# Kernel optimization log

Hardware: AMD Instinct MI355X
Metric: run time of the kernel (lower is better)

The kernel has to match this reference:

```python
import jax, jax.numpy as jnp
import numpy as np

EMBED_DIM = 1024
NUM_HEADS = 16
HEAD_DIM = EMBED_DIM // NUM_HEADS
SCALE = HEAD_DIM ** -0.5


def setup_inputs() -> dict:
    key = jax.random.key(0)
    k1, k2, k3, k4, k5, k6 = jax.random.split(key, 6)
    B, Tq, Tk = 2, 2048, 2048
    std = EMBED_DIM ** -0.5
    return {
        "x_q": jax.random.normal(k1, (B, Tq, EMBED_DIM), jnp.float32),
        "x_kv": jax.random.normal(k2, (B, Tk, EMBED_DIM), jnp.float32),
        "w_q": jax.random.normal(k3, (EMBED_DIM, EMBED_DIM), jnp.float32) * std,
        "w_kv": jax.random.normal(k4, (EMBED_DIM, 2 * EMBED_DIM), jnp.float32) * std,
        "w_proj": jax.random.normal(k5, (EMBED_DIM, EMBED_DIM), jnp.float32) * std,
        "w_rel": jax.random.normal(k6, (1, NUM_HEADS), jnp.float32) * 0.02,
    }


def reference(x_q, x_kv, w_q, w_kv, w_proj, w_rel):
    B, Tq, _ = x_q.shape
    Tk = x_kv.shape[1]
    # projections
    q = x_q @ w_q                       # [B,Tq,E]
    kv = x_kv @ w_kv                    # [B,Tk,2E]
    k, v = jnp.split(kv, 2, axis=-1)

    def heads(y, T):
        return y.reshape(B, T, NUM_HEADS, HEAD_DIM).transpose(0, 2, 1, 3)

    q = heads(q, Tq)                    # [B,H,Tq,D]
    k = heads(k, Tk)
    v = heads(v, Tk)

    logits = jnp.einsum('bhqd,bhkd->bhqk', q, k) * SCALE  # [B,H,Tq,Tk]

    # relative position bias: Dense(1 -> H) applied to (pos_q - pos_k)
    rel = jnp.arange(Tq, dtype=jnp.float32)[:, None] - jnp.arange(Tk, dtype=jnp.float32)[None, :]
    bias = rel[..., None] * w_rel[0]                      # [Tq,Tk,H]
    bias = bias.transpose(2, 0, 1)[None]                  # [1,H,Tq,Tk]
    logits = logits + bias

    attn = jax.nn.softmax(logits, axis=-1)                # dropout=0 / inference -> identity
    out = jnp.einsum('bhqk,bhkd->bhqd', attn, v)          # [B,H,Tq,D]
    out = out.transpose(0, 2, 1, 3).reshape(B, Tq, EMBED_DIM)
    return out @ w_proj
```

## Files before the change

kernel.cpp:

```cpp
#include <hip/hip_runtime.h>
#include <hip/hip_bf16.h>

typedef __attribute__((ext_vector_type(8))) short short8;
typedef __attribute__((ext_vector_type(8))) __bf16 bf16x8;
typedef __attribute__((ext_vector_type(4))) float f32x4;
typedef __attribute__((ext_vector_type(8))) unsigned short ushort8v;
typedef __attribute__((ext_vector_type(4))) unsigned short ushort4v;

#define NB 2
#define TQ 2048
#define TKK 2048
#define EMB 1024
#define NH 16
#define HD 64

__device__ __forceinline__ unsigned short f2bf(float f){
  union { float f; unsigned u; } v; v.f = f;
  unsigned r = v.u + 0x7FFFu + ((v.u >> 16) & 1u);
  return (unsigned short)(r >> 16);
}

#define GLOAD_LDS16(g, l) __builtin_amdgcn_global_load_lds( \
    (const __attribute__((address_space(1))) void*)(g), \
    (__attribute__((address_space(3))) void*)(l), 16, 0, 0)

#define SWZ(row, inner) ((inner) ^ (((row)&7)<<4))

__device__ __forceinline__ void mfma16(const short8& a, const short8& b, f32x4& c){
  c = __builtin_amdgcn_mfma_f32_16x16x32_bf16(
        __builtin_bit_cast(bf16x8, a), __builtin_bit_cast(bf16x8, b), c, 0, 0, 0);
}

__device__ __forceinline__ void cvt_body(const float* __restrict__ in,
    unsigned short* __restrict__ out, int i){
  float4 v = ((const float4*)in)[i];
  ushort4v o;
  o.x = f2bf(v.x); o.y = f2bf(v.y); o.z = f2bf(v.z); o.w = f2bf(v.w);
  ((ushort4v*)out)[i] = o;
}

__device__ __forceinline__ void wt_body(const float* __restrict__ W,
    unsigned short* __restrict__ WT, int K, int N, int k0, int n0,
    unsigned short (*tile)[72]){
  int tid = threadIdx.x;
  #pragma unroll
  for (int it=0; it<4; ++it){
    int c = tid + it*256;
    int r = c>>4, c4 = (c&15)*4;
    float4 v = *(const float4*)(W + (long)(k0+r)*N + n0 + c4);
    tile[r][c4+0]=f2bf(v.x); tile[r][c4+1]=f2bf(v.y);
    tile[r][c4+2]=f2bf(v.z); tile[r][c4+3]=f2bf(v.w);
  }
  __syncthreads();
  #pragma unroll
  for (int it=0; it<2; ++it){
    int c = tid + it*256;
    int n = c>>3, k8 = (c&7)*8;
    ushort8v o;
    #pragma unroll
    for (int j=0;j<8;++j) o[j] = tile[k8+j][n];
    *(ushort8v*)(WT + (long)(n0+n)*K + k0 + k8) = o;
  }
}

__global__ __launch_bounds__(256) void prep_kernel(
    const float* __restrict__ x_q, const float* __restrict__ x_kv,
    const float* __restrict__ w_q, const float* __restrict__ w_kv,
    const float* __restrict__ w_proj,
    unsigned short* __restrict__ Aq,  unsigned short* __restrict__ Akv,
    unsigned short* __restrict__ WqT, unsigned short* __restrict__ WkvT,
    unsigned short* __restrict__ WpT){
  __shared__ unsigned short tile[64][72];
  const int bx = blockIdx.x;
  if (bx < 4096){
    cvt_body(x_q, Aq, bx*256 + threadIdx.x);
  } else if (bx < 8192){
    cvt_body(x_kv, Akv, (bx-4096)*256 + threadIdx.x);
  } else if (bx < 8448){
    int blk = bx - 8192;
    wt_body(w_q, WqT, EMB, EMB, (blk>>4)*64, (blk&15)*64, tile);
  } else if (bx < 8960){
    int blk = bx - 8448;
    wt_body(w_kv, WkvT, EMB, 2*EMB, (blk>>5)*64, (blk&31)*64, tile);
  } else {
    int blk = bx - 8960;
    wt_body(w_proj, WpT, EMB, EMB, (blk>>4)*64, (blk&15)*64, tile);
  }
}

template<int MODE>
__device__ __forceinline__ void gemm_body(const unsigned short* __restrict__ A,
    const unsigned short* __restrict__ BT, void* __restrict__ Cout,
    int M, int N, int K, int m0, int n0,
    unsigned short* Al, unsigned short* Bl, const float* __restrict__ w_rel){
  const int tid = threadIdx.x;
  const int wave = tid>>6, lane = tid&63;
  const int wm = (wave>>1)*64, wn = (wave&1)*64;
  const int g = lane>>4, lr = lane&15;
  const int srow = lane>>3;
  const int sinner = (lane&7)*16;
  f32x4 acc[4][4] = {};

  for (int k0=0; k0<K; k0+=64){
    #pragma unroll
    for (int j=0;j<4;++j){
      int chunk = wave*4 + j;
      int row = chunk*8 + srow;
      int kb = SWZ(row, sinner);
      GLOAD_LDS16(A + (long)(m0+row)*K + k0 + (kb>>1), Al + chunk*512);
      GLOAD_LDS16(BT + (long)(n0+row)*K + k0 + (kb>>1), Bl + chunk*512);
    }
    __syncthreads();
    #pragma unroll
    for (int kk=0;kk<2;++kk){
      short8 af[4], bfr[4];
      const int kbyte = kk*64 + g*16;
      #pragma unroll
      for (int i=0;i<4;++i){
        int ar = wm + i*16 + lr;
        af[i] = *(const short8*)((const char*)Al + ar*128 + SWZ(ar, kbyte));
        int br = wn + i*16 + lr;
        bfr[i] = *(const short8*)((const char*)Bl + br*128 + SWZ(br, kbyte));
      }
      #pragma unroll
      for (int i=0;i<4;++i)
        #pragma unroll
        for (int jn=0;jn<4;++jn)
          mfma16(af[i], bfr[jn], acc[i][jn]);
    }
    __syncthreads();
  }
  #pragma unroll
  for (int i=0;i<4;++i){
    int row = m0 + wm + i*16 + g*4;
    #pragma unroll
    for (int jn=0;jn<4;++jn){
      if (MODE == 2){
        int dg = n0 - EMB + wn + jn*16 + lr;
        int h = dg >> 6, d = dg & 63;
        int b = row >> 11, t = row & (TKK-1);
        float wr2h = w_rel[h]*1.44269504f;
        float fac = exp2f(-(float)(t & 63)*wr2h);
        float stp = exp2f(-wr2h);
        ushort4v w;
        #pragma unroll
        for (int r=0;r<4;++r){ w[r] = f2bf(acc[i][jn][r]*fac); fac *= stp; }
        *(ushort4v*)((unsigned short*)Cout + ((long)((b*NH + h)*HD + d)*TKK + t)) = w;
      } else {
        int col = n0 + wn + jn*16 + lr;
        #pragma unroll
        for (int r=0;r<4;++r){
          if (MODE == 1)
            ((unsigned short*)Cout)[(long)(row+r)*N + col] = f2bf(acc[i][jn][r]);
          else
            ((float*)Cout)[(long)(row+r)*N + col] = acc[i][jn][r];
        }
      }
    }
  }
}

__global__ __launch_bounds__(256,3) void gemm_qkv(
    const unsigned short* __restrict__ Aq,  const unsigned short* __restrict__ WqT,  unsigned short* __restrict__ Qb,
    const unsigned short* __restrict__ Akv, const unsigned short* __restrict__ WkvT,
    unsigned short* __restrict__ Kb, unsigned short* __restrict__ VT,
    const float* __restrict__ w_rel){
  __shared__ unsigned short Al[128*64];
  __shared__ unsigned short Bl[128*64];
  const int p = blockIdx.x + 24*blockIdx.y;
  const int x = (p & 7) + 8*((p >> 3) % 3);
  const int y = (p >> 3) / 3;
  if (x < 8)
    gemm_body<1>(Aq,  WqT,  Qb, NB*TQ, EMB, EMB, y*128, x*128, Al, Bl, nullptr);
  else if (x < 16)
    gemm_body<1>(Akv, WkvT, Kb, NB*TKK, EMB, EMB, y*128, (x-8)*128, Al, Bl, nullptr);
  else
    gemm_body<2>(Akv, WkvT, VT, NB*TKK, EMB, EMB, y*128, EMB + (x-16)*128, Al, Bl, w_rel);
}

__global__ __launch_bounds__(256,2) void gemm_out(const unsigned short* __restrict__ A,
    const unsigned short* __restrict__ BT, float* __restrict__ C,
    int M, int N, int K){
  __shared__ unsigned short Al[64*64];
  __shared__ unsigned short Bl[128*64];
  const int tid = threadIdx.x;
  const int wave = tid>>6, lane = tid&63;
  const int m0 = blockIdx.y*64, n0 = blockIdx.x*128;
  const int wm = (wave>>1)*32, wn = (wave&1)*64;
  const int g = lane>>4, lr = lane&15;
  const int srow = lane>>3;
  const int sinner = (lane&7)*16;
  f32x4 acc[2][4] = {};

  for (int k0=0; k0<K; k0+=64){
    #pragma unroll
    for (int j=0;j<2;++j){
      int chunk = wave*2 + j;
      int row = chunk*8 + srow;
      int kb = SWZ(row, sinner);
      GLOAD_LDS16(A + (long)(m0+row)*K + k0 + (kb>>1), Al + chunk*512);
    }
    #pragma unroll
    for (int j=0;j<4;++j){
      int chunk = wave*4 + j;
      int row = chunk*8 + srow;
      int kb = SWZ(row, sinner);
      GLOAD_LDS16(BT + (long)(n0+row)*K + k0 + (kb>>1), Bl + chunk*512);
    }
    __syncthreads();
    #pragma unroll
    for (int kk=0;kk<2;++kk){
      short8 af[2], bfr[4];
      const int kbyte = kk*64 + g*16;
      #pragma unroll
      for (int i=0;i<2;++i){
        int ar = wm + i*16 + lr;
        af[i] = *(const short8*)((const char*)Al + ar*128 + SWZ(ar, kbyte));
      }
      #pragma unroll
      for (int jn=0;jn<4;++jn){
        int br = wn + jn*16 + lr;
        bfr[jn] = *(const short8*)((const char*)Bl + br*128 + SWZ(br, kbyte));
      }
      #pragma unroll
      for (int i=0;i<2;++i)
        #pragma unroll
        for (int jn=0;jn<4;++jn)
          mfma16(af[i], bfr[jn], acc[i][jn]);
    }
    __syncthreads();
  }
  #pragma unroll
  for (int i=0;i<2;++i){
    int row = m0 + wm + i*16 + g*4;
    #pragma unroll
    for (int jn=0;jn<4;++jn){
      int col = n0 + wn + jn*16 + lr;
      #pragma unroll
      for (int r=0;r<4;++r)
        C[(long)(row+r)*N + col] = acc[i][jn][r];
    }
  }
}

__global__ __launch_bounds__(512,4) void attn_kernel(const unsigned short* __restrict__ Qb,
    const unsigned short* __restrict__ Kb, const unsigned short* __restrict__ VT,
    const float* __restrict__ w_rel, unsigned short* __restrict__ Ob){
  __shared__ unsigned short Kl[3][64*64];
  __shared__ unsigned short Vl[3][64*64];
  __shared__ __attribute__((aligned(16))) char Pl[8][16*128];
  const int id  = blockIdx.x + 16*blockIdx.y;
  const int nid = (id & 7)*64 + (id >> 3);
  const int qb  = nid & 15, bh = nid >> 4;
  const int b = bh>>4, h = bh&15;
  const int q0 = qb*128;
  const int tid = threadIdx.x, wave = tid>>6, lane = tid&63;
  const int g = lane>>4, lr = lane&15;
  const int srow = lane>>3, sinner = (lane&7)*16;
  const float C1 = 0.125f*1.44269504f;
  const float wr2 = w_rel[h]*1.44269504f;
  const float w64 = 64.0f*wr2;
  char* Pw = &Pl[wave][0];

  const int strow = wave*8 + srow;
  const int skb = SWZ(strow, sinner);
  const unsigned short* Kg = Kb + (long)(b*TKK + strow)*EMB + h*HD + (skb>>1);
  const unsigned short* Vg = VT + (long)(bh*HD + strow)*TKK + (skb>>1);

  short8 qf[2];
  #pragma unroll
  for (int kk=0;kk<2;++kk)
    qf[kk] = *(const short8*)(Qb + (long)(b*TQ + q0 + wave*16 + lr)*EMB + h*HD + kk*32 + g*8);

  short8 cfrag[2];
  #pragma unroll
  for (int kk=0;kk<2;++kk)
    #pragma unroll
    for (int j=0;j<8;++j)
      cfrag[kk][j] = (short)f2bf(exp2f(-(float)(kk*32 + g*8 + j)*wr2));

  f32x4 oacc[4] = {};
  f32x4 lacc = {};
  float Mxs = -1e30f;

  GLOAD_LDS16(Kg, &Kl[0][wave*512]);
  GLOAD_LDS16(Vg, &Vl[0][wave*512]);
  GLOAD_LDS16(Kg + (long)64*EMB, &Kl[1][wave*512]);
  GLOAD_LDS16(Vg + 64, &Vl[1][wave*512]);
  asm volatile("s_waitcnt vmcnt(2)" ::: "memory");
  __builtin_amdgcn_s_barrier();

  int cur = 0;
  for (int kt=0; kt<TKK; kt+=64){
    const bool issue = (kt + 128 < TKK);
    int nxt2 = cur + 2; if (nxt2 >= 3) nxt2 -= 3;
    if (issue){
      GLOAD_LDS16(Kg + (long)(kt+128)*EMB, &Kl[nxt2][wave*512]);
      GLOAD_LDS16(Vg + (kt+128), &Vl[nxt2][wave*512]);
    }

    f32x4 sacc[4] = {};
    __builtin_amdgcn_s_setprio(1);
    #pragma unroll
    for (int kk=0;kk<2;++kk){
      short8 kf[4];
      const int kbyte = kk*64 + g*16;
      #pragma unroll
      for (int n=0;n<4;++n){
        int trow = n*16 + lr;
        kf[n] = *(const short8*)((const char*)&Kl[cur][0] + trow*128 + SWZ(trow, kbyte));
      }
      #pragma unroll
      for (int n=0;n<4;++n)
        mfma16(kf[n], qf[kk], sacc[n]);
    }
    __builtin_amdgcn_s_setprio(0);

    float rowmax;
    {
      float m0 = fmaxf(fmaxf(sacc[0][0],sacc[0][1]),sacc[0][2]);
      float m1 = fmaxf(fmaxf(sacc[0][3],sacc[1][0]),sacc[1][1]);
      float m2 = fmaxf(fmaxf(sacc[1][2],sacc[1][3]),sacc[2][0]);
      float m3 = fmaxf(fmaxf(sacc[2][1],sacc[2][2]),sacc[2][3]);
      float m4 = fmaxf(fmaxf(sacc[3][0],sacc[3][1]),sacc[3][2]);
      float a  = fmaxf(fmaxf(m0,m1),m2);
      float bb = fmaxf(fmaxf(m3,m4),sacc[3][3]);
      rowmax = fmaxf(a,bb);
      rowmax = fmaxf(rowmax, __shfl_xor(rowmax, 16, 64));
      rowmax = fmaxf(rowmax, __shfl_xor(rowmax, 32, 64));
    }
    float rowmax_s = rowmax*C1;

    if (__any(rowmax_s > Mxs + 8.0f)){
      float Mn = fmaxf(Mxs, rowmax_s);
      float rf = exp2f(Mxs - Mn);
      Mxs = Mn;
      float rfo[4];
      #pragma unroll
      for (int r=0;r<4;++r) rfo[r] = __shfl(rf, 4*g + r, 64);
      #pragma unroll
      for (int n=0;n<4;++n)
        #pragma unroll
        for (int r=0;r<4;++r) oacc[n][r] *= rfo[r];
      #pragma unroll
      for (int r=0;r<4;++r) lacc[r] *= rfo[r];
    }

    #pragma unroll
    for (int n=0;n<4;++n){
      ushort4v w;
      #pragma unroll
      for (int r=0;r<4;++r)
        w[r] = __builtin_bit_cast(unsigned short,
                 __float2bfloat16(exp2f(fmaf(sacc[n][r], C1, -Mxs))));
      *(ushort4v*)(Pw + lr*128 + SWZ(lr, 32*n + 8*g)) = w;
    }

    asm volatile("" ::: "memory");

    __builtin_amdgcn_s_setprio(1);
    #pragma unroll
    for (int kk=0;kk<2;++kk){
      const int kbyte = kk*64 + g*16;
      short8 pf = *(const short8*)(Pw + lr*128 + SWZ(lr, kbyte));
      #pragma unroll
      for (int n=0;n<4;++n){
        int vrow = n*16 + lr;
        short8 vf = *(const short8*)((const char*)&Vl[cur][0] + vrow*128 + SWZ(vrow, kbyte));
        mfma16(pf, vf, oacc[n]);
      }
      mfma16(pf, cfrag[kk], lacc);
    }
    __builtin_amdgcn_s_setprio(0);

    Mxs += w64;

    if (issue) asm volatile("s_waitcnt vmcnt(2) lgkmcnt(0)" ::: "memory");
    else       asm volatile("s_waitcnt vmcnt(0) lgkmcnt(0)" ::: "memory");
    __builtin_amdgcn_s_barrier();
    cur += 1; if (cur >= 3) cur -= 3;
  }

  #pragma unroll
  for (int r=0;r<4;++r){
    float inv = 1.0f / lacc[r];
    int q = q0 + wave*16 + 4*g + r;
    #pragma unroll
    for (int n=0;n<4;++n){
      int d = n*16 + lr;
      Ob[(long)(b*TQ + q)*EMB + h*HD + d] = f2bf(oacc[n][r]*inv);
    }
  }
}

extern "C" void kernel_launch(void* const* d_in, const int* in_sizes, int n_in,
                              void* d_out, int out_size, void* d_ws, size_t ws_size,
                              hipStream_t stream){
  const float* x_q    = (const float*)d_in[0];
  const float* x_kv   = (const float*)d_in[1];
  const float* w_q    = (const float*)d_in[2];
  const float* w_kv   = (const float*)d_in[3];
  const float* w_proj = (const float*)d_in[4];
  const float* w_rel  = (const float*)d_in[5];
  (void)in_sizes; (void)n_in; (void)out_size; (void)ws_size;
  char* ws = (char*)d_ws;
  const size_t MB = 1024*1024;
  unsigned short* Qb   = (unsigned short*)(ws + 0);
  unsigned short* Kb   = (unsigned short*)(ws + 8*MB);
  unsigned short* VT   = (unsigned short*)(ws + 16*MB);
  unsigned short* WpT  = (unsigned short*)(ws + 24*MB);
  unsigned short* WqT  = (unsigned short*)(ws + 26*MB);
  unsigned short* WkvT = (unsigned short*)(ws + 28*MB);
  unsigned short* Aq   = (unsigned short*)(ws + 32*MB);
  unsigned short* Akv  = (unsigned short*)(ws + 40*MB);
  unsigned short* Ob   = Aq;
  float* out = (float*)d_out;

  prep_kernel<<<9216, 256, 0, stream>>>(x_q, x_kv, w_q, w_kv, w_proj,
                                        Aq, Akv, WqT, WkvT, WpT);
  gemm_qkv<<<dim3(24,32), 256, 0, stream>>>(Aq, WqT, Qb, Akv, WkvT, Kb, VT, w_rel);
  attn_kernel<<<dim3(16,32), 512, 0, stream>>>(Qb, Kb, VT, w_rel, Ob);
  gemm_out<<<dim3(8,64), 256, 0, stream>>>(Ob, WpT, out, NB*TQ, EMB, EMB);
}
```

Before: 144.6 us.

## Give each attention wave two 16-row query tiles to reuse K/V fragments

The attention block now runs 4 waves of 256 threads instead of 8, and each wave handles 32 query rows as two 16-row tiles. Each K and V fragment read from LDS feeds two MFMAs, which halves LDS traffic per MFMA. Online softmax state is duplicated per tile, and each wave now issues twice as many global-to-LDS loads. The cost is more registers per wave and fewer waves per block, so latency hiding and occupancy may suffer.

```diff
diff --git a/kernel.cpp b/kernel.cpp
--- a/kernel.cpp
+++ b/kernel.cpp
@@ -243,12 +243,12 @@
   }
 }
 
-__global__ __launch_bounds__(512,4) void attn_kernel(const unsigned short* __restrict__ Qb,
+__global__ __launch_bounds__(256,2) void attn_kernel(const unsigned short* __restrict__ Qb,
     const unsigned short* __restrict__ Kb, const unsigned short* __restrict__ VT,
     const float* __restrict__ w_rel, unsigned short* __restrict__ Ob){
   __shared__ unsigned short Kl[3][64*64];
   __shared__ unsigned short Vl[3][64*64];
-  __shared__ __attribute__((aligned(16))) char Pl[8][16*128];
+  __shared__ __attribute__((aligned(16))) char Pl[4][32*128];
   const int id  = blockIdx.x + 16*blockIdx.y;
   const int nid = (id & 7)*64 + (id >> 3);
   const int qb  = nid & 15, bh = nid >> 4;
@@ -262,15 +262,19 @@
   const float w64 = 64.0f*wr2;
   char* Pw = &Pl[wave][0];
 
-  const int strow = wave*8 + srow;
+  const int strow = wave*16 + srow;
   const int skb = SWZ(strow, sinner);
-  const unsigned short* Kg = Kb + (long)(b*TKK + strow)*EMB + h*HD + (skb>>1);
-  const unsigned short* Vg = VT + (long)(bh*HD + strow)*TKK + (skb>>1);
-
-  short8 qf[2];
-  #pragma unroll
-  for (int kk=0;kk<2;++kk)
-    qf[kk] = *(const short8*)(Qb + (long)(b*TQ + q0 + wave*16 + lr)*EMB + h*HD + kk*32 + g*8);
+  const unsigned short* Kg  = Kb + (long)(b*TKK + strow)*EMB + h*HD + (skb>>1);
+  const unsigned short* Vg  = VT + (long)(bh*HD + strow)*TKK + (skb>>1);
+  const unsigned short* Kg2 = Kg + (long)8*EMB;
+  const unsigned short* Vg2 = Vg + (long)8*TKK;
+
+  short8 qf[2][2];
+  #pragma unroll
+  for (int m=0;m<2;++m)
+    #pragma unroll
+    for (int kk=0;kk<2;++kk)
+      qf[m][kk] = *(const short8*)(Qb + (long)(b*TQ + q0 + wave*32 + m*16 + lr)*EMB + h*HD + kk*32 + g*8);
 
   short8 cfrag[2];
   #pragma unroll
@@ -279,15 +283,19 @@
     for (int j=0;j<8;++j)
       cfrag[kk][j] = (short)f2bf(exp2f(-(float)(kk*32 + g*8 + j)*wr2));
 
-  f32x4 oacc[4] = {};
-  f32x4 lacc = {};
-  float Mxs = -1e30f;
-
-  GLOAD_LDS16(Kg, &Kl[0][wave*512]);
-  GLOAD_LDS16(Vg, &Vl[0][wave*512]);
-  GLOAD_LDS16(Kg + (long)64*EMB, &Kl[1][wave*512]);
-  GLOAD_LDS16(Vg + 64, &Vl[1][wave*512]);
-  asm volatile("s_waitcnt vmcnt(2)" ::: "memory");
+  f32x4 oacc[2][4] = {};
+  f32x4 lacc[2] = {};
+  float Mxs[2] = {-1e30f, -1e30f};
+
+  GLOAD_LDS16(Kg,  &Kl[0][wave*1024]);
+  GLOAD_LDS16(Kg2, &Kl[0][wave*1024+512]);
+  GLOAD_LDS16(Vg,  &Vl[0][wave*1024]);
+  GLOAD_LDS16(Vg2, &Vl[0][wave*1024+512]);
+  GLOAD_LDS16(Kg  + (long)64*EMB, &Kl[1][wave*1024]);
+  GLOAD_LDS16(Kg2 + (long)64*EMB, &Kl[1][wave*1024+512]);
+  GLOAD_LDS16(Vg  + 64, &Vl[1][wave*1024]);
+  GLOAD_LDS16(Vg2 + 64, &Vl[1][wave*1024+512]);
+  asm volatile("s_waitcnt vmcnt(4)" ::: "memory");
   __builtin_amdgcn_s_barrier();
 
   int cur = 0;
@@ -295,11 +303,13 @@
     const bool issue = (kt + 128 < TKK);
     int nxt2 = cur + 2; if (nxt2 >= 3) nxt2 -= 3;
     if (issue){
-      GLOAD_LDS16(Kg + (long)(kt+128)*EMB, &Kl[nxt2][wave*512]);
-      GLOAD_LDS16(Vg + (kt+128), &Vl[nxt2][wave*512]);
-    }
-
-    f32x4 sacc[4] = {};
+      GLOAD_LDS16(Kg  + (long)(kt+128)*EMB, &Kl[nxt2][wave*1024]);
+      GLOAD_LDS16(Kg2 + (long)(kt+128)*EMB, &Kl[nxt2][wave*1024+512]);
+      GLOAD_LDS16(Vg  + (kt+128), &Vl[nxt2][wave*1024]);
+      GLOAD_LDS16(Vg2 + (kt+128), &Vl[nxt2][wave*1024+512]);
+    }
+
+    f32x4 sacc[2][4] = {};
     __builtin_amdgcn_s_setprio(1);
     #pragma unroll
     for (int kk=0;kk<2;++kk){
@@ -312,49 +322,58 @@
       }
       #pragma unroll
       for (int n=0;n<4;++n)
-        mfma16(kf[n], qf[kk], sacc[n]);
+        #pragma unroll
+        for (int m=0;m<2;++m)
+          mfma16(kf[n], qf[m][kk], sacc[m][n]);
     }
     __builtin_amdgcn_s_setprio(0);
 
-    float rowmax;
-    {
-      float m0 = fmaxf(fmaxf(sacc[0][0],sacc[0][1]),sacc[0][2]);
-      float m1 = fmaxf(fmaxf(sacc[0][3],sacc[1][0]),sacc[1][1]);
-      float m2 = fmaxf(fmaxf(sacc[1][2],sacc[1][3]),sacc[2][0]);
-      float m3 = fmaxf(fmaxf(sacc[2][1],sacc[2][2]),sacc[2][3]);
-      float m4 = fmaxf(fmaxf(sacc[3][0],sacc[3][1]),sacc[3][2]);
+    float rs[2];
+    #pragma unroll
+    for (int m=0;m<2;++m){
+      float m0 = fmaxf(fmaxf(sacc[m][0][0],sacc[m][0][1]),sacc[m][0][2]);
+      float m1 = fmaxf(fmaxf(sacc[m][0][3],sacc[m][1][0]),sacc[m][1][1]);
+      float m2 = fmaxf(fmaxf(sacc[m][1][2],sacc[m][1][3]),sacc[m][2][0]);
+      float m3 = fmaxf(fmaxf(sacc[m][2][1],sacc[m][2][2]),sacc[m][2][3]);
+      float m4 = fmaxf(fmaxf(sacc[m][3][0],sacc[m][3][1]),sacc[m][3][2]);
       float a  = fmaxf(fmaxf(m0,m1),m2);
-      float bb = fmaxf(fmaxf(m3,m4),sacc[3][3]);
-      rowmax = fmaxf(a,bb);
+      float bb = fmaxf(fmaxf(m3,m4),sacc[m][3][3]);
+      float rowmax = fmaxf(a,bb);
       rowmax = fmaxf(rowmax, __shfl_xor(rowmax, 16, 64));
       rowmax = fmaxf(rowmax, __shfl_xor(rowmax, 32, 64));
-    }
-    float rowmax_s = rowmax*C1;
-
-    if (__any(rowmax_s > Mxs + 8.0f)){
-      float Mn = fmaxf(Mxs, rowmax_s);
-      float rf = exp2f(Mxs - Mn);
-      Mxs = Mn;
-      float rfo[4];
-      #pragma unroll
-      for (int r=0;r<4;++r) rfo[r] = __shfl(rf, 4*g + r, 64);
-      #pragma unroll
-      for (int n=0;n<4;++n)
-        #pragma unroll
-        for (int r=0;r<4;++r) oacc[n][r] *= rfo[r];
-      #pragma unroll
-      for (int r=0;r<4;++r) lacc[r] *= rfo[r];
-    }
-
-    #pragma unroll
-    for (int n=0;n<4;++n){
-      ushort4v w;
-      #pragma unroll
-      for (int r=0;r<4;++r)
-        w[r] = __builtin_bit_cast(unsigned short,
-                 __float2bfloat16(exp2f(fmaf(sacc[n][r], C1, -Mxs))));
-      *(ushort4v*)(Pw + lr*128 + SWZ(lr, 32*n + 8*g)) = w;
-    }
+      rs[m] = rowmax*C1;
+    }
+
+    int grew = (rs[0] > Mxs[0] + 8.0f) | (rs[1] > Mxs[1] + 8.0f);
+    if (__any(grew)){
+      #pragma unroll
+      for (int m=0;m<2;++m){
+        float Mn = fmaxf(Mxs[m], rs[m]);
+        float rf = exp2f(Mxs[m] - Mn);
+        Mxs[m] = Mn;
+        float rfo[4];
+        #pragma unroll
+        for (int r=0;r<4;++r) rfo[r] = __shfl(rf, 4*g + r, 64);
+        #pragma unroll
+        for (int n=0;n<4;++n)
+          #pragma unroll
+          for (int r=0;r<4;++r) oacc[m][n][r] *= rfo[r];
+        #pragma unroll
+        for (int r=0;r<4;++r) lacc[m][r] *= rfo[r];
+      }
+    }
+
+    #pragma unroll
+    for (int m=0;m<2;++m)
+      #pragma unroll
+      for (int n=0;n<4;++n){
+        ushort4v w;
+        #pragma unroll
+        for (int r=0;r<4;++r)
+          w[r] = __builtin_bit_cast(unsigned short,
+                   __float2bfloat16(exp2f(fmaf(sacc[m][n][r], C1, -Mxs[m]))));
+        *(ushort4v*)(Pw + (m*16+lr)*128 + SWZ(lr, 32*n + 8*g)) = w;
+      }
 
     asm volatile("" ::: "memory");
 
@@ -362,35 +381,44 @@
     #pragma unroll
     for (int kk=0;kk<2;++kk){
       const int kbyte = kk*64 + g*16;
-      short8 pf = *(const short8*)(Pw + lr*128 + SWZ(lr, kbyte));
+      short8 pf[2];
+      #pragma unroll
+      for (int m=0;m<2;++m)
+        pf[m] = *(const short8*)(Pw + (m*16+lr)*128 + SWZ(lr, kbyte));
       #pragma unroll
       for (int n=0;n<4;++n){
         int vrow = n*16 + lr;
         short8 vf = *(const short8*)((const char*)&Vl[cur][0] + vrow*128 + SWZ(vrow, kbyte));
-        mfma16(pf, vf, oacc[n]);
-      }
-      mfma16(pf, cfrag[kk], lacc);
+        #pragma unroll
+        for (int m=0;m<2;++m)
+          mfma16(pf[m], vf, oacc[m][n]);
+      }
+      #pragma unroll
+      for (int m=0;m<2;++m)
+        mfma16(pf[m], cfrag[kk], lacc[m]);
     }
     __builtin_amdgcn_s_setprio(0);
 
-    Mxs += w64;
-
-    if (issue) asm volatile("s_waitcnt vmcnt(2) lgkmcnt(0)" ::: "memory");
+    Mxs[0] += w64; Mxs[1] += w64;
+
+    if (issue) asm volatile("s_waitcnt vmcnt(4) lgkmcnt(0)" ::: "memory");
     else       asm volatile("s_waitcnt vmcnt(0) lgkmcnt(0)" ::: "memory");
     __builtin_amdgcn_s_barrier();
     cur += 1; if (cur >= 3) cur -= 3;
   }
 
   #pragma unroll
-  for (int r=0;r<4;++r){
-    float inv = 1.0f / lacc[r];
-    int q = q0 + wave*16 + 4*g + r;
-    #pragma unroll
-    for (int n=0;n<4;++n){
-      int d = n*16 + lr;
-      Ob[(long)(b*TQ + q)*EMB + h*HD + d] = f2bf(oacc[n][r]*inv);
-    }
-  }
+  for (int m=0;m<2;++m)
+    #pragma unroll
+    for (int r=0;r<4;++r){
+      float inv = 1.0f / lacc[m][r];
+      int q = q0 + wave*32 + m*16 + 4*g + r;
+      #pragma unroll
+      for (int n=0;n<4;++n){
+        int d = n*16 + lr;
+        Ob[(long)(b*TQ + q)*EMB + h*HD + d] = f2bf(oacc[m][n][r]*inv);
+      }
+    }
 }
 
 extern "C" void kernel_launch(void* const* d_in, const int* in_sizes, int n_in,
@@ -419,6 +447,6 @@
   prep_kernel<<<9216, 256, 0, stream>>>(x_q, x_kv, w_q, w_kv, w_proj,
                                         Aq, Akv, WqT, WkvT, WpT);
   gemm_qkv<<<dim3(24,32), 256, 0, stream>>>(Aq, WqT, Qb, Akv, WkvT, Kb, VT, w_rel);
-  attn_kernel<<<dim3(16,32), 512, 0, stream>>>(Qb, Kb, VT, w_rel, Ob);
+  attn_kernel<<<dim3(16,32), 256, 0, stream>>>(Qb, Kb, VT, w_rel, Ob);
   gemm_out<<<dim3(8,64), 256, 0, stream>>>(Ob, WpT, out, NB*TQ, EMB, EMB);
 }
```

Result: no change. 147.3 us (+1.9%).

## Process 128-key tiles per iteration with double buffering instead of triple

Applied to the files above, without the earlier changes.

Replaces the 3-stage ring of 64-key K/V tiles with a 2-stage double buffer whose slots each hold two 64-key halves, so each loop iteration handles 128 keys. This halves the number of barriers and waitcnt points and amortizes the running-max check over two half-tiles, adjusting the per-half bias shift. The cost is a less deep prefetch: each iteration now waits for all outstanding loads (vmcnt(0)), which can expose memory latency. It also adds register pressure from the doubled score accumulators.

```diff
diff --git a/kernel.cpp b/kernel.cpp
--- a/kernel.cpp
+++ b/kernel.cpp
@@ -246,8 +246,8 @@
 __global__ __launch_bounds__(512,4) void attn_kernel(const unsigned short* __restrict__ Qb,
     const unsigned short* __restrict__ Kb, const unsigned short* __restrict__ VT,
     const float* __restrict__ w_rel, unsigned short* __restrict__ Ob){
-  __shared__ unsigned short Kl[3][64*64];
-  __shared__ unsigned short Vl[3][64*64];
+  __shared__ unsigned short Kl[2][2][64*64];
+  __shared__ unsigned short Vl[2][2][64*64];
   __shared__ __attribute__((aligned(16))) char Pl[8][16*128];
   const int id  = blockIdx.x + 16*blockIdx.y;
   const int nid = (id & 7)*64 + (id >> 3);
@@ -283,56 +283,60 @@
   f32x4 lacc = {};
   float Mxs = -1e30f;
 
-  GLOAD_LDS16(Kg, &Kl[0][wave*512]);
-  GLOAD_LDS16(Vg, &Vl[0][wave*512]);
-  GLOAD_LDS16(Kg + (long)64*EMB, &Kl[1][wave*512]);
-  GLOAD_LDS16(Vg + 64, &Vl[1][wave*512]);
-  asm volatile("s_waitcnt vmcnt(2)" ::: "memory");
+  GLOAD_LDS16(Kg,                 &Kl[0][0][wave*512]);
+  GLOAD_LDS16(Kg + (long)64*EMB,  &Kl[0][1][wave*512]);
+  GLOAD_LDS16(Vg,                 &Vl[0][0][wave*512]);
+  GLOAD_LDS16(Vg + 64,            &Vl[0][1][wave*512]);
+  asm volatile("s_waitcnt vmcnt(0)" ::: "memory");
   __builtin_amdgcn_s_barrier();
 
   int cur = 0;
-  for (int kt=0; kt<TKK; kt+=64){
-    const bool issue = (kt + 128 < TKK);
-    int nxt2 = cur + 2; if (nxt2 >= 3) nxt2 -= 3;
-    if (issue){
-      GLOAD_LDS16(Kg + (long)(kt+128)*EMB, &Kl[nxt2][wave*512]);
-      GLOAD_LDS16(Vg + (kt+128), &Vl[nxt2][wave*512]);
-    }
-
-    f32x4 sacc[4] = {};
+  for (int kt=0; kt<TKK; kt+=128){
+    if (kt + 128 < TKK){
+      GLOAD_LDS16(Kg + (long)(kt+128)*EMB,    &Kl[cur^1][0][wave*512]);
+      GLOAD_LDS16(Kg + (long)(kt+192)*EMB,    &Kl[cur^1][1][wave*512]);
+      GLOAD_LDS16(Vg + (kt+128),              &Vl[cur^1][0][wave*512]);
+      GLOAD_LDS16(Vg + (kt+192),              &Vl[cur^1][1][wave*512]);
+    }
+
+    f32x4 sacc[2][4] = {};
     __builtin_amdgcn_s_setprio(1);
     #pragma unroll
-    for (int kk=0;kk<2;++kk){
-      short8 kf[4];
-      const int kbyte = kk*64 + g*16;
-      #pragma unroll
-      for (int n=0;n<4;++n){
-        int trow = n*16 + lr;
-        kf[n] = *(const short8*)((const char*)&Kl[cur][0] + trow*128 + SWZ(trow, kbyte));
-      }
-      #pragma unroll
-      for (int n=0;n<4;++n)
-        mfma16(kf[n], qf[kk], sacc[n]);
-    }
+    for (int hf=0;hf<2;++hf)
+      #pragma unroll
+      for (int kk=0;kk<2;++kk){
+        short8 kf[4];
+        const int kbyte = kk*64 + g*16;
+        #pragma unroll
+        for (int n=0;n<4;++n){
+          int trow = n*16 + lr;
+          kf[n] = *(const short8*)((const char*)&Kl[cur][hf][0] + trow*128 + SWZ(trow, kbyte));
+        }
+        #pragma unroll
+        for (int n=0;n<4;++n)
+          mfma16(kf[n], qf[kk], sacc[hf][n]);
+      }
     __builtin_amdgcn_s_setprio(0);
 
-    float rowmax;
-    {
-      float m0 = fmaxf(fmaxf(sacc[0][0],sacc[0][1]),sacc[0][2]);
-      float m1 = fmaxf(fmaxf(sacc[0][3],sacc[1][0]),sacc[1][1]);
-      float m2 = fmaxf(fmaxf(sacc[1][2],sacc[1][3]),sacc[2][0]);
-      float m3 = fmaxf(fmaxf(sacc[2][1],sacc[2][2]),sacc[2][3]);
-      float m4 = fmaxf(fmaxf(sacc[3][0],sacc[3][1]),sacc[3][2]);
+    float rs[2];
+    #pragma unroll
+    for (int hf=0;hf<2;++hf){
+      float m0 = fmaxf(fmaxf(sacc[hf][0][0],sacc[hf][0][1]),sacc[hf][0][2]);
+      float m1 = fmaxf(fmaxf(sacc[hf][0][3],sacc[hf][1][0]),sacc[hf][1][1]);
+      float m2 = fmaxf(fmaxf(sacc[hf][1][2],sacc[hf][1][3]),sacc[hf][2][0]);
+      float m3 = fmaxf(fmaxf(sacc[hf][2][1],sacc[hf][2][2]),sacc[hf][2][3]);
+      float m4 = fmaxf(fmaxf(sacc[hf][3][0],sacc[hf][3][1]),sacc[hf][3][2]);
       float a  = fmaxf(fmaxf(m0,m1),m2);
-      float bb = fmaxf(fmaxf(m3,m4),sacc[3][3]);
-      rowmax = fmaxf(a,bb);
+      float bb = fmaxf(fmaxf(m3,m4),sacc[hf][3][3]);
+      float rowmax = fmaxf(a,bb);
       rowmax = fmaxf(rowmax, __shfl_xor(rowmax, 16, 64));
       rowmax = fmaxf(rowmax, __shfl_xor(rowmax, 32, 64));
-    }
-    float rowmax_s = rowmax*C1;
-
-    if (__any(rowmax_s > Mxs + 8.0f)){
-      float Mn = fmaxf(Mxs, rowmax_s);
+      rs[hf] = rowmax*C1;
+    }
+
+    int grew = (rs[0] > Mxs + 8.0f) | (rs[1] > Mxs + w64 + 8.0f);
+    if (__any(grew)){
+      float Mn = fmaxf(Mxs, fmaxf(rs[0], rs[1] - w64));
       float rf = exp2f(Mxs - Mn);
       Mxs = Mn;
       float rfo[4];
@@ -347,38 +351,40 @@
     }
 
     #pragma unroll
-    for (int n=0;n<4;++n){
-      ushort4v w;
-      #pragma unroll
-      for (int r=0;r<4;++r)
-        w[r] = __builtin_bit_cast(unsigned short,
-                 __float2bfloat16(exp2f(fmaf(sacc[n][r], C1, -Mxs))));
-      *(ushort4v*)(Pw + lr*128 + SWZ(lr, 32*n + 8*g)) = w;
-    }
-
-    asm volatile("" ::: "memory");
-
-    __builtin_amdgcn_s_setprio(1);
-    #pragma unroll
-    for (int kk=0;kk<2;++kk){
-      const int kbyte = kk*64 + g*16;
-      short8 pf = *(const short8*)(Pw + lr*128 + SWZ(lr, kbyte));
+    for (int hf=0;hf<2;++hf){
+      const float mshift = (hf == 0) ? Mxs : (Mxs + w64);
       #pragma unroll
       for (int n=0;n<4;++n){
-        int vrow = n*16 + lr;
-        short8 vf = *(const short8*)((const char*)&Vl[cur][0] + vrow*128 + SWZ(vrow, kbyte));
-        mfma16(pf, vf, oacc[n]);
-      }
-      mfma16(pf, cfrag[kk], lacc);
-    }
-    __builtin_amdgcn_s_setprio(0);
-
-    Mxs += w64;
-
-    if (issue) asm volatile("s_waitcnt vmcnt(2) lgkmcnt(0)" ::: "memory");
-    else       asm volatile("s_waitcnt vmcnt(0) lgkmcnt(0)" ::: "memory");
+        ushort4v w;
+        #pragma unroll
+        for (int r=0;r<4;++r)
+          w[r] = __builtin_bit_cast(unsigned short,
+                   __float2bfloat16(exp2f(fmaf(sacc[hf][n][r], C1, -mshift))));
+        *(ushort4v*)(Pw + lr*128 + SWZ(lr, 32*n + 8*g)) = w;
+      }
+      asm volatile("" ::: "memory");
+      __builtin_amdgcn_s_setprio(1);
+      #pragma unroll
+      for (int kk=0;kk<2;++kk){
+        const int kbyte = kk*64 + g*16;
+        short8 pf = *(const short8*)(Pw + lr*128 + SWZ(lr, kbyte));
+        #pragma unroll
+        for (int n=0;n<4;++n){
+          int vrow = n*16 + lr;
+          short8 vf = *(const short8*)((const char*)&Vl[cur][hf][0] + vrow*128 + SWZ(vrow, kbyte));
+          mfma16(pf, vf, oacc[n]);
+        }
+        mfma16(pf, cfrag[kk], lacc);
+      }
+      __builtin_amdgcn_s_setprio(0);
+      asm volatile("" ::: "memory");
+    }
+
+    Mxs += 2.0f*w64;
+
+    asm volatile("s_waitcnt vmcnt(0) lgkmcnt(0)" ::: "memory");
     __builtin_amdgcn_s_barrier();
-    cur += 1; if (cur >= 3) cur -= 3;
+    cur ^= 1;
   }
 
   #pragma unroll
```

Result: faster. 141.6 us (median of 2 runs) (-2.1%).
